# Optimization experiments

Hardware: AMD Instinct MI355X
Metric: run time of the kernel (lower is better)

## Reference

```python
import jax, jax.numpy as jnp
import numpy as np

HIDDEN = 2048
NUM_HEADS = 32
NUM_KV_HEADS = 8
HEAD_DIM = HIDDEN // NUM_HEADS  # 64


def setup_inputs() -> dict:
    key = jax.random.key(0)
    ks = jax.random.split(key, 5)
    s = 0.02
    x = jax.random.normal(ks[0], (2, 2048, HIDDEN), dtype=jnp.float32)
    Wq = jax.random.normal(ks[1], (HIDDEN, NUM_HEADS * HEAD_DIM), dtype=jnp.float32) * s
    Wk = jax.random.normal(ks[2], (HIDDEN, NUM_KV_HEADS * HEAD_DIM), dtype=jnp.float32) * s
    Wv = jax.random.normal(ks[3], (HIDDEN, NUM_KV_HEADS * HEAD_DIM), dtype=jnp.float32) * s
    Wo = jax.random.normal(ks[4], (NUM_HEADS * HEAD_DIM, HIDDEN), dtype=jnp.float32) * s
    return {"x": x, "Wq": Wq, "Wk": Wk, "Wv": Wv, "Wo": Wo}


def reference(x, Wq, Wk, Wv, Wo):
    b, s, _ = x.shape
    # projections: [b, s, h, d] -> [b, h, s, d]
    q = (x @ Wq).reshape(b, s, NUM_HEADS, HEAD_DIM).transpose(0, 2, 1, 3)
    k = (x @ Wk).reshape(b, s, NUM_KV_HEADS, HEAD_DIM).transpose(0, 2, 1, 3)
    v = (x @ Wv).reshape(b, s, NUM_KV_HEADS, HEAD_DIM).transpose(0, 2, 1, 3)
    rep = NUM_HEADS // NUM_KV_HEADS
    # repeat_interleave along head dim (consecutive copies), matching torch
    k = jnp.repeat(k, rep, axis=1)
    v = jnp.repeat(v, rep, axis=1)
    scale = HEAD_DIM ** (-0.5)
    attn = jnp.einsum("bhqd,bhkd->bhqk", q, k) * scale  # [b,h,s,s]
    attn = jax.nn.softmax(attn, axis=-1)
    out = jnp.einsum("bhqk,bhkd->bhqd", attn, v)
    out = out.transpose(0, 2, 1, 3).reshape(b, s, NUM_HEADS * HEAD_DIM)
    return out @ Wo
```

## Files before the change

kernel.cpp:

```cpp
#include <hip/hip_runtime.h>

typedef __attribute__((ext_vector_type(8))) short short8;
typedef __attribute__((ext_vector_type(4))) float f32x4;
typedef __attribute__((ext_vector_type(4))) unsigned short u16x4;
typedef __attribute__((ext_vector_type(8))) unsigned short u16x8;

__device__ __forceinline__ unsigned short f2bf(float f) {
  union { float f; unsigned u; } v; v.f = f;
  unsigned r = v.u + 0x7FFFu + ((v.u >> 16) & 1u);
  return (unsigned short)(r >> 16);
}

#define GLL16(g, l) \
  __builtin_amdgcn_global_load_lds((const __attribute__((address_space(1))) void*)(g), \
                                   (__attribute__((address_space(3))) void*)(l), 16, 0, 0)

__global__ __launch_bounds__(256) void cvt_x_kernel(const float* __restrict__ in,
                                                    unsigned short* __restrict__ out) {
  const int i = blockIdx.x * 256 + threadIdx.x;
  const f32x4* p = (const f32x4*)in;
  f32x4 a = p[2 * i], b = p[2 * i + 1];
  u16x8 r;
  r[0] = f2bf(a[0]); r[1] = f2bf(a[1]); r[2] = f2bf(a[2]); r[3] = f2bf(a[3]);
  r[4] = f2bf(b[0]); r[5] = f2bf(b[1]); r[6] = f2bf(b[2]); r[7] = f2bf(b[3]);
  ((u16x8*)out)[i] = r;
}

__global__ __launch_bounds__(256) void tpose_kernel(const float* __restrict__ in,
                                                    unsigned short* __restrict__ out,
                                                    int R, int C, int ldo) {
  __shared__ float tile[32][33];
  const int c0 = blockIdx.x * 32, r0 = blockIdx.y * 32;
  const int tx = threadIdx.x & 31, ty = threadIdx.x >> 5;
#pragma unroll
  for (int i = 0; i < 4; ++i)
    tile[ty + i * 8][tx] = in[(size_t)(r0 + ty + i * 8) * C + c0 + tx];
  __syncthreads();
#pragma unroll
  for (int i = 0; i < 4; ++i)
    out[(size_t)(c0 + ty + i * 8) * ldo + r0 + tx] = f2bf(tile[tx][ty + i * 8]);
}

__global__ __launch_bounds__(256) void gemm_qkv_kernel(const unsigned short* __restrict__ A,
                                                       const unsigned short* __restrict__ BT,
                                                       unsigned short* __restrict__ Cq,
                                                       unsigned short* __restrict__ VT) {
  __shared__ unsigned short As[2][128 * 32];
  __shared__ unsigned short Bs[2][128 * 32];
  const int tid = threadIdx.x;
  const int wave = tid >> 6, lane = tid & 63;
  const int r16 = lane & 15, g = lane >> 4;
  const int n0 = blockIdx.x * 128, m0 = blockIdx.y * 128;
  const int wr = wave >> 1, wc = wave & 1;
  f32x4 acc[4][4] = {};
  const int so = wave * 1024 + lane * 16;

  auto STAGE = [&](int kt, int bufi) {
    const int k0 = kt * 32;
#pragma unroll
    for (int i = 0; i < 2; ++i) {
      const int o = i * 4096 + so;
      const int row = o >> 6;
      const int ke = (o & 63) >> 1;
      GLL16(A + (size_t)(m0 + row) * 2048 + k0 + ke, (char*)As[bufi] + i * 4096 + wave * 1024);
      GLL16(BT + (size_t)(n0 + row) * 2048 + k0 + ke, (char*)Bs[bufi] + i * 4096 + wave * 1024);
    }
  };
  STAGE(0, 0);
  __syncthreads();
  for (int kt = 0; kt < 64; ++kt) {
    const int cur = kt & 1;
    if (kt < 63) STAGE(kt + 1, cur ^ 1);
    short8 af[4], bfr[4];
#pragma unroll
    for (int mi = 0; mi < 4; ++mi) {
      const int row = wr * 64 + mi * 16 + r16;
      af[mi] = *(const short8*)((const char*)As[cur] + row * 64 + g * 16);
    }
#pragma unroll
    for (int ni = 0; ni < 4; ++ni) {
      const int row = wc * 64 + ni * 16 + r16;
      bfr[ni] = *(const short8*)((const char*)Bs[cur] + row * 64 + g * 16);
    }
#pragma unroll
    for (int mi = 0; mi < 4; ++mi)
#pragma unroll
      for (int ni = 0; ni < 4; ++ni)
        acc[mi][ni] = __builtin_amdgcn_mfma_f32_16x16x32_bf16(af[mi], bfr[ni], acc[mi][ni], 0, 0, 0);
    __syncthreads();
  }
  const float qs = 0.18033688f;
#pragma unroll
  for (int mi = 0; mi < 4; ++mi) {
#pragma unroll
    for (int ni = 0; ni < 4; ++ni) {
      const int n = n0 + wc * 64 + ni * 16 + r16;
      const int mb = m0 + wr * 64 + mi * 16 + g * 4;
      f32x4 v = acc[mi][ni];
      if (n < 2560) {
        const float s = (n < 2048) ? qs : 1.0f;
#pragma unroll
        for (int r = 0; r < 4; ++r) Cq[(size_t)(mb + r) * 3072 + n] = f2bf(v[r] * s);
      } else {
        const int d = n - 2560;
        const int bb = mb >> 11, s0 = mb & 2047;
        u16x4 pk;
#pragma unroll
        for (int r = 0; r < 4; ++r) pk[r] = f2bf(v[r]);
        *(u16x4*)(VT + (size_t)(bb * 512 + d) * 2048 + s0) = pk;
      }
    }
  }
}

__global__ __launch_bounds__(256) void gemm_out_kernel(const unsigned short* __restrict__ A,
                                                       const unsigned short* __restrict__ BT,
                                                       float* __restrict__ Co) {
  __shared__ unsigned short As[2][128 * 32];
  __shared__ unsigned short Bs[2][128 * 32];
  const int tid = threadIdx.x;
  const int wave = tid >> 6, lane = tid & 63;
  const int r16 = lane & 15, g = lane >> 4;
  const int n0 = blockIdx.x * 128, m0 = blockIdx.y * 128;
  const int wr = wave >> 1, wc = wave & 1;
  f32x4 acc[4][4] = {};
  const int so = wave * 1024 + lane * 16;

  auto STAGE = [&](int kt, int bufi) {
    const int k0 = kt * 32;
#pragma unroll
    for (int i = 0; i < 2; ++i) {
      const int o = i * 4096 + so;
      const int row = o >> 6;
      const int ke = (o & 63) >> 1;
      GLL16(A + (size_t)(m0 + row) * 2048 + k0 + ke, (char*)As[bufi] + i * 4096 + wave * 1024);
      GLL16(BT + (size_t)(n0 + row) * 2048 + k0 + ke, (char*)Bs[bufi] + i * 4096 + wave * 1024);
    }
  };
  STAGE(0, 0);
  __syncthreads();
  for (int kt = 0; kt < 64; ++kt) {
    const int cur = kt & 1;
    if (kt < 63) STAGE(kt + 1, cur ^ 1);
    short8 af[4], bfr[4];
#pragma unroll
    for (int mi = 0; mi < 4; ++mi) {
      const int row = wr * 64 + mi * 16 + r16;
      af[mi] = *(const short8*)((const char*)As[cur] + row * 64 + g * 16);
    }
#pragma unroll
    for (int ni = 0; ni < 4; ++ni) {
      const int row = wc * 64 + ni * 16 + r16;
      bfr[ni] = *(const short8*)((const char*)Bs[cur] + row * 64 + g * 16);
    }
#pragma unroll
    for (int mi = 0; mi < 4; ++mi)
#pragma unroll
      for (int ni = 0; ni < 4; ++ni)
        acc[mi][ni] = __builtin_amdgcn_mfma_f32_16x16x32_bf16(af[mi], bfr[ni], acc[mi][ni], 0, 0, 0);
    __syncthreads();
  }
#pragma unroll
  for (int mi = 0; mi < 4; ++mi)
#pragma unroll
    for (int ni = 0; ni < 4; ++ni) {
      const int n = n0 + wc * 64 + ni * 16 + r16;
      const int mb = m0 + wr * 64 + mi * 16 + g * 4;
      f32x4 v = acc[mi][ni];
#pragma unroll
      for (int r = 0; r < 4; ++r) Co[(size_t)(mb + r) * 2048 + n] = v[r];
    }
}

__global__ __launch_bounds__(256) void attn_kernel(const unsigned short* __restrict__ QKV,
                                                   const unsigned short* __restrict__ VT,
                                                   unsigned short* __restrict__ O) {
  __shared__ unsigned short Ks[2][64 * 64];
  __shared__ unsigned short Vs[2][64 * 64];
  const int tid = threadIdx.x;
  const int wave = tid >> 6, lane = tid & 63;
  const int r16 = lane & 15, g = lane >> 4;
  const int qt = blockIdx.x, bh = blockIdx.y;
  const int b = bh >> 5, h = bh & 31, kvh = h >> 2;
  const int qtok0 = b * 2048 + qt * 128 + wave * 32;
  short8 qf[2][2];
#pragma unroll
  for (int mt = 0; mt < 2; ++mt)
#pragma unroll
    for (int kh = 0; kh < 2; ++kh)
      qf[mt][kh] = *(const short8*)(QKV + (size_t)(qtok0 + mt * 16 + r16) * 3072 + h * 64 + kh * 32 + g * 8);
  f32x4 oa[2][4] = {};
  float lsum[2] = {0.f, 0.f};
  const unsigned short* Kb = QKV + (size_t)b * 2048 * 3072 + 2048 + kvh * 64;
  const unsigned short* Vb = VT + (size_t)(b * 512 + kvh * 64) * 2048;
  const int so = wave * 1024 + lane * 16;

  auto STAGE = [&](int t, int bufi) {
    const int kv0 = t * 64;
#pragma unroll
    for (int i = 0; i < 2; ++i) {
      const int o = i * 4096 + so;
      const int row = o >> 7;
      const int c = ((((o >> 4) & 7) ^ (row & 7))) * 8;
      GLL16(Kb + (size_t)(kv0 + row) * 3072 + c, (char*)Ks[bufi] + i * 4096 + wave * 1024);
      GLL16(Vb + (size_t)row * 2048 + kv0 + c, (char*)Vs[bufi] + i * 4096 + wave * 1024);
    }
  };
  STAGE(0, 0);
  __syncthreads();
  for (int t = 0; t < 32; ++t) {
    const int cur = t & 1;
    if (t < 31) STAGE(t + 1, cur ^ 1);
    f32x4 sc[2][4];
    __builtin_amdgcn_s_setprio(1);
#pragma unroll
    for (int jt = 0; jt < 4; ++jt) {
      short8 kf0, kf1;
      const int j = jt * 16 + r16;
      kf0 = *(const short8*)((const char*)Ks[cur] + j * 128 + ((g * 16) ^ ((j & 7) << 4)));
      kf1 = *(const short8*)((const char*)Ks[cur] + j * 128 + ((64 + g * 16) ^ ((j & 7) << 4)));
#pragma unroll
      for (int mt = 0; mt < 2; ++mt) {
        f32x4 z = {0.f, 0.f, 0.f, 0.f};
        z = __builtin_amdgcn_mfma_f32_16x16x32_bf16(kf0, qf[mt][0], z, 0, 0, 0);
        z = __builtin_amdgcn_mfma_f32_16x16x32_bf16(kf1, qf[mt][1], z, 0, 0, 0);
        sc[mt][jt] = z;
      }
    }
    __builtin_amdgcn_s_setprio(0);
    short8 pa[2][2];
#pragma unroll
    for (int mt = 0; mt < 2; ++mt) {
      unsigned pk[4][2];
#pragma unroll
      for (int jt = 0; jt < 4; ++jt) {
        float p0 = __builtin_amdgcn_exp2f(sc[mt][jt][0] - 8.0f);
        float p1 = __builtin_amdgcn_exp2f(sc[mt][jt][1] - 8.0f);
        float p2 = __builtin_amdgcn_exp2f(sc[mt][jt][2] - 8.0f);
        float p3 = __builtin_amdgcn_exp2f(sc[mt][jt][3] - 8.0f);
        lsum[mt] += (p0 + p1) + (p2 + p3);
        asm("v_cvt_pk_bf16_f32 %0, %1, %2" : "=v"(pk[jt][0]) : "v"(p0), "v"(p1));
        asm("v_cvt_pk_bf16_f32 %0, %1, %2" : "=v"(pk[jt][1]) : "v"(p2), "v"(p3));
      }
#pragma unroll
      for (int kh = 0; kh < 2; ++kh) {
        union { unsigned u[4]; short8 s; } pu;
        pu.u[0] = pk[2 * kh][0]; pu.u[1] = pk[2 * kh][1];
        pu.u[2] = pk[2 * kh + 1][0]; pu.u[3] = pk[2 * kh + 1][1];
        pa[mt][kh] = pu.s;
      }
    }
    __builtin_amdgcn_s_setprio(1);
#pragma unroll
    for (int dt = 0; dt < 4; ++dt) {
      const int d = dt * 16 + r16;
      const char* vrow = (const char*)Vs[cur] + d * 128;
      const int sw = (d & 7) << 4;
#pragma unroll
      for (int kh = 0; kh < 2; ++kh) {
        u16x4 va = *(const u16x4*)(vrow + ((kh * 64 + 8 * g) ^ sw));
        u16x4 vb2 = *(const u16x4*)(vrow + ((kh * 64 + 32 + 8 * g) ^ sw));
        union { u16x4 h[2]; short8 s; } vu;
        vu.h[0] = va; vu.h[1] = vb2;
#pragma unroll
        for (int mt = 0; mt < 2; ++mt)
          oa[mt][dt] = __builtin_amdgcn_mfma_f32_16x16x32_bf16(pa[mt][kh], vu.s, oa[mt][dt], 0, 0, 0);
      }
    }
    __builtin_amdgcn_s_setprio(0);
    __syncthreads();
  }
  float inv[2][4];
#pragma unroll
  for (int mt = 0; mt < 2; ++mt) {
    float l = lsum[mt];
    l += __shfl_xor(l, 16);
    l += __shfl_xor(l, 32);
#pragma unroll
    for (int r = 0; r < 4; ++r)
      inv[mt][r] = 1.0f / __shfl(l, (lane & 48) | (((lane >> 4) & 3) * 4 + r));
  }
#pragma unroll
  for (int mt = 0; mt < 2; ++mt)
#pragma unroll
    for (int dt = 0; dt < 4; ++dt)
#pragma unroll
      for (int r = 0; r < 4; ++r)
        O[(size_t)(qtok0 + mt * 16 + g * 4 + r) * 2048 + h * 64 + dt * 16 + r16] =
            f2bf(oa[mt][dt][r] * inv[mt][r]);
}

extern "C" void kernel_launch(void* const* d_in, const int* in_sizes, int n_in,
                              void* d_out, int out_size, void* d_ws, size_t ws_size,
                              hipStream_t stream) {
  const float* x  = (const float*)d_in[0];
  const float* Wq = (const float*)d_in[1];
  const float* Wk = (const float*)d_in[2];
  const float* Wv = (const float*)d_in[3];
  const float* Wo = (const float*)d_in[4];
  char* w = (char*)d_ws;
  unsigned short* xb    = (unsigned short*)(w);
  unsigned short* wqkvt = (unsigned short*)(w + 16777216);
  unsigned short* wot   = (unsigned short*)(w + 29360128);
  unsigned short* qkv   = (unsigned short*)(w + 37748736);
  unsigned short* vt    = (unsigned short*)(w + 62914560);
  unsigned short* ob    = (unsigned short*)(w + 67108864);
  float* out = (float*)d_out;

  cvt_x_kernel<<<4096, 256, 0, stream>>>(x, xb);
  tpose_kernel<<<dim3(64, 64), 256, 0, stream>>>(Wq, wqkvt, 2048, 2048, 2048);
  tpose_kernel<<<dim3(16, 64), 256, 0, stream>>>(Wk, wqkvt + (size_t)2048 * 2048, 2048, 512, 2048);
  tpose_kernel<<<dim3(16, 64), 256, 0, stream>>>(Wv, wqkvt + (size_t)2560 * 2048, 2048, 512, 2048);
  tpose_kernel<<<dim3(64, 64), 256, 0, stream>>>(Wo, wot, 2048, 2048, 2048);
  gemm_qkv_kernel<<<dim3(24, 32), 256, 0, stream>>>(xb, wqkvt, qkv, vt);
  attn_kernel<<<dim3(16, 64), 256, 0, stream>>>(qkv, vt, ob);
  gemm_out_kernel<<<dim3(16, 32), 256, 0, stream>>>(ob, wot, out);
}
```

Before: 257.4 us.

## Fold softmax offset into MFMA init, compute row sums via MFMA, permute V layout

The -8 exponent offset moves into the initial accumulator of the QK MFMA, so the per-element subtraction disappears. The row-sum of probabilities is now computed with extra MFMAs against a vector of bf16 ones, replacing the scalar adds and the cross-lane shuffle reduction at the end. The transposed-V store is also permuted within 32-token groups so the PV operand can be read with one 16-byte LDS load instead of two 8-byte loads. In exchange each tile issues four extra MFMAs, and the row sums are taken over bf16-rounded probabilities rather than fp32 values.

New measurement: 242.8 us. -5.7%, faster.

```diff
diff --git a/kernel.cpp b/kernel.cpp
--- a/kernel.cpp
+++ b/kernel.cpp
@@ -104,10 +104,11 @@
       } else {
         const int d = n - 2560;
         const int bb = mb >> 11, s0 = mb & 2047;
+        const int s0p = (s0 & ~31) | (((s0 >> 2) & 3) << 3) | (((s0 >> 4) & 1) << 2);
         u16x4 pk;
 #pragma unroll
         for (int r = 0; r < 4; ++r) pk[r] = f2bf(v[r]);
-        *(u16x4*)(VT + (size_t)(bb * 512 + d) * 2048 + s0) = pk;
+        *(u16x4*)(VT + (size_t)(bb * 512 + d) * 2048 + s0p) = pk;
       }
     }
   }
@@ -189,8 +190,10 @@
 #pragma unroll
     for (int kh = 0; kh < 2; ++kh)
       qf[mt][kh] = *(const short8*)(QKV + (size_t)(qtok0 + mt * 16 + r16) * 3072 + h * 64 + kh * 32 + g * 8);
+  union { unsigned u[4]; short8 s; } ones;
+  ones.u[0] = ones.u[1] = ones.u[2] = ones.u[3] = 0x3F803F80u;
   f32x4 oa[2][4] = {};
-  float lsum[2] = {0.f, 0.f};
+  f32x4 lacc[2] = {};
   const unsigned short* Kb = QKV + (size_t)b * 2048 * 3072 + 2048 + kvh * 64;
   const unsigned short* Vb = VT + (size_t)(b * 512 + kvh * 64) * 2048;
   const int so = wave * 1024 + lane * 16;
@@ -221,7 +224,7 @@
       kf1 = *(const short8*)((const char*)Ks[cur] + j * 128 + ((64 + g * 16) ^ ((j & 7) << 4)));
 #pragma unroll
       for (int mt = 0; mt < 2; ++mt) {
-        f32x4 z = {0.f, 0.f, 0.f, 0.f};
+        f32x4 z = {-8.f, -8.f, -8.f, -8.f};
         z = __builtin_amdgcn_mfma_f32_16x16x32_bf16(kf0, qf[mt][0], z, 0, 0, 0);
         z = __builtin_amdgcn_mfma_f32_16x16x32_bf16(kf1, qf[mt][1], z, 0, 0, 0);
         sc[mt][jt] = z;
@@ -234,11 +237,10 @@
       unsigned pk[4][2];
 #pragma unroll
       for (int jt = 0; jt < 4; ++jt) {
-        float p0 = __builtin_amdgcn_exp2f(sc[mt][jt][0] - 8.0f);
-        float p1 = __builtin_amdgcn_exp2f(sc[mt][jt][1] - 8.0f);
-        float p2 = __builtin_amdgcn_exp2f(sc[mt][jt][2] - 8.0f);
-        float p3 = __builtin_amdgcn_exp2f(sc[mt][jt][3] - 8.0f);
-        lsum[mt] += (p0 + p1) + (p2 + p3);
+        float p0 = __builtin_amdgcn_exp2f(sc[mt][jt][0]);
+        float p1 = __builtin_amdgcn_exp2f(sc[mt][jt][1]);
+        float p2 = __builtin_amdgcn_exp2f(sc[mt][jt][2]);
+        float p3 = __builtin_amdgcn_exp2f(sc[mt][jt][3]);
         asm("v_cvt_pk_bf16_f32 %0, %1, %2" : "=v"(pk[jt][0]) : "v"(p0), "v"(p1));
         asm("v_cvt_pk_bf16_f32 %0, %1, %2" : "=v"(pk[jt][1]) : "v"(p2), "v"(p3));
       }
@@ -252,34 +254,26 @@
     }
     __builtin_amdgcn_s_setprio(1);
 #pragma unroll
+    for (int mt = 0; mt < 2; ++mt) {
+      lacc[mt] = __builtin_amdgcn_mfma_f32_16x16x32_bf16(pa[mt][0], ones.s, lacc[mt], 0, 0, 0);
+      lacc[mt] = __builtin_amdgcn_mfma_f32_16x16x32_bf16(pa[mt][1], ones.s, lacc[mt], 0, 0, 0);
+    }
+#pragma unroll
     for (int dt = 0; dt < 4; ++dt) {
       const int d = dt * 16 + r16;
       const char* vrow = (const char*)Vs[cur] + d * 128;
       const int sw = (d & 7) << 4;
 #pragma unroll
       for (int kh = 0; kh < 2; ++kh) {
-        u16x4 va = *(const u16x4*)(vrow + ((kh * 64 + 8 * g) ^ sw));
-        u16x4 vb2 = *(const u16x4*)(vrow + ((kh * 64 + 32 + 8 * g) ^ sw));
-        union { u16x4 h[2]; short8 s; } vu;
-        vu.h[0] = va; vu.h[1] = vb2;
+        short8 vf = *(const short8*)(vrow + ((kh * 64 + g * 16) ^ sw));
 #pragma unroll
         for (int mt = 0; mt < 2; ++mt)
-          oa[mt][dt] = __builtin_amdgcn_mfma_f32_16x16x32_bf16(pa[mt][kh], vu.s, oa[mt][dt], 0, 0, 0);
+          oa[mt][dt] = __builtin_amdgcn_mfma_f32_16x16x32_bf16(pa[mt][kh], vf, oa[mt][dt], 0, 0, 0);
       }
     }
     __builtin_amdgcn_s_setprio(0);
     __syncthreads();
   }
-  float inv[2][4];
-#pragma unroll
-  for (int mt = 0; mt < 2; ++mt) {
-    float l = lsum[mt];
-    l += __shfl_xor(l, 16);
-    l += __shfl_xor(l, 32);
-#pragma unroll
-    for (int r = 0; r < 4; ++r)
-      inv[mt][r] = 1.0f / __shfl(l, (lane & 48) | (((lane >> 4) & 3) * 4 + r));
-  }
 #pragma unroll
   for (int mt = 0; mt < 2; ++mt)
 #pragma unroll
@@ -287,7 +281,7 @@
 #pragma unroll
       for (int r = 0; r < 4; ++r)
         O[(size_t)(qtok0 + mt * 16 + g * 4 + r) * 2048 + h * 64 + dt * 16 + r16] =
-            f2bf(oa[mt][dt][r] * inv[mt][r]);
+            f2bf(oa[mt][dt][r] / lacc[mt][r]);
 }
 
 extern "C" void kernel_launch(void* const* d_in, const int* in_sizes, int n_in,
```
